# Kernel tuning notes

Measured on AMD Instinct MI355X. Metric: run time of the kernel, lower is better.

Reference implementation:

```python
import jax, jax.numpy as jnp
import numpy as np


def _embedding_distances(dictionary, x_flat):
    # dictionary: [D, C], x_flat: [T, C] -> [T, D]
    dict_norms = jnp.sum(dictionary * dictionary, axis=-1)          # [D]
    x_norms = jnp.sum(x_flat * x_flat, axis=-1)                     # [T]
    dots = jnp.einsum('tc,dc->td', x_flat, dictionary)              # [T, D]
    return -2.0 * dots + dict_norms[None, :] + x_norms[:, None]


def _quantize(x, dictionary):
    # x: [N, C, H, W]
    N, C, H, W = x.shape
    cl = jnp.transpose(x, (0, 2, 3, 1))                             # [N, H, W, C]
    diffs = _embedding_distances(dictionary, cl.reshape(-1, C))     # [NHW, D]
    idxs = jnp.argmin(diffs, axis=-1).reshape(N, H, W)              # [N, H, W]
    embedded = jnp.transpose(dictionary[idxs], (0, 3, 1, 2))        # [N, C, H, W]
    embedded_pt = jax.lax.stop_gradient(embedded) + (x - jax.lax.stop_gradient(x))
    return embedded, embedded_pt, idxs


def setup_inputs() -> dict:
    key = jax.random.key(0)
    k1, k2, k3 = jax.random.split(key, 3)
    N, C, H, W, D = 32, 256, 32, 32, 1024
    return {
        'inputs': jax.random.normal(k1, (N, C, H, W), dtype=jnp.float32),
        'inputs_thermal': jax.random.normal(k2, (N, C, H, W), dtype=jnp.float32),
        'dictionary': jax.random.normal(k3, (D, C), dtype=jnp.float32),
    }


def reference(inputs, inputs_thermal, dictionary):
    embedded, embedded_pt, idxs = _quantize(inputs, dictionary)
    embedded_t, embedded_pt_t, idxs_t = _quantize(inputs_thermal, dictionary)
    return (embedded, embedded_pt, idxs, embedded_t, embedded_pt_t, idxs_t)
```

## Files before the change

kernel.cpp:

```cpp
#include <hip/hip_runtime.h>

#define NB    32
#define CCH   256
#define HW    1024
#define NPIX  (NB*HW)
#define DDICT 1024

#define EMB_ELEMS  ((size_t)NB*CCH*HW)
#define SEC_ELEMS  (2*EMB_ELEMS + NPIX)

#define TPX  256
#define TD   128
#define NDT  (DDICT/TD)
#define BK   32
#define NKC  (CCH/BK)
#define NPH  (NDT*NKC)

#define TAU  0.125f

typedef __attribute__((ext_vector_type(8))) short bf16x8;
typedef __attribute__((ext_vector_type(4))) float f32x4;

__device__ inline ushort split_rne(float f, float& rest) {
    uint u = __float_as_uint(f);
    uint r = u + 0x7FFFu + ((u >> 16) & 1u);
    rest = f - __uint_as_float(r & 0xFFFF0000u);
    return (ushort)(r >> 16);
}

__device__ inline ushort rne_bf16(float f) {
    uint u = __float_as_uint(f);
    return (ushort)((u + 0x7FFFu + ((u >> 16) & 1u)) >> 16);
}

__device__ inline void gll16(const void* g, void* l) {
    __builtin_amdgcn_global_load_lds(
        (const __attribute__((address_space(1))) uint*)g,
        (__attribute__((address_space(3))) uint*)l,
        16, 0, 0);
}

__device__ inline void nts16(float* p, float a, float b, float c, float d) {
    f32x4 v = {a, b, c, d};
    __builtin_nontemporal_store(v, (f32x4*)p);
}

__global__ void dict_norms_kernel(const float* __restrict__ dict,
                                  float* __restrict__ norms,
                                  int* __restrict__ cnts) {
    if (blockIdx.x == 0 && threadIdx.x < 2) cnts[threadIdx.x] = 0;
    int d = blockIdx.x * blockDim.x + threadIdx.x;
    if (d < DDICT) {
        const float4* row = (const float4*)(dict + (size_t)d * CCH);
        float s = 0.f;
#pragma unroll 8
        for (int i = 0; i < CCH / 4; ++i) {
            float4 v = row[i];
            s += v.x * v.x + v.y * v.y + v.z * v.z + v.w * v.w;
        }
        norms[d] = s;
    }
}

__global__ void dict_split_kernel(const float* __restrict__ dict,
                                  ushort* __restrict__ dHs,
                                  ushort* __restrict__ dMs,
                                  float* __restrict__ dictT) {
    int d = blockIdx.x;
    int lane = threadIdx.x;
    float4 f = ((const float4*)(dict + (size_t)d * CCH))[lane];
    float v[4] = {f.x, f.y, f.z, f.w};
    ushort h[4], m[4];
#pragma unroll
    for (int i = 0; i < 4; ++i) {
        float r1;
        h[i] = split_rne(v[i], r1);
        m[i] = rne_bf16(r1);
    }
    int c0 = lane * 4;
    int kc = c0 >> 5, oct = (c0 >> 3) & 3, e0 = c0 & 7;
    int dt = d >> 7, dd = d & 127;
    int slot = (oct + (dd >> 1)) & 3;
    size_t base = ((size_t)(dt * NKC + kc)) * 4096 + dd * 32 + slot * 8 + e0;
    *(ushort4*)(dHs + base) = make_ushort4(h[0], h[1], h[2], h[3]);
    *(ushort4*)(dMs + base) = make_ushort4(m[0], m[1], m[2], m[3]);
#pragma unroll
    for (int j = 0; j < 4; ++j)
        dictT[(size_t)(c0 + j) * DDICT + d] = v[j];
}

__global__ __launch_bounds__(512, 1)
void vq_mfma_kernel(const float* __restrict__ x0,
                    const float* __restrict__ x1,
                    const ushort* __restrict__ dHs,
                    const ushort* __restrict__ dMs,
                    const float* __restrict__ norms,
                    const float* __restrict__ dict,
                    float* __restrict__ out,
                    int* __restrict__ cnts,
                    int* __restrict__ lists) {
    __shared__ ushort Bs[2][2][4096];
    __shared__ float nrm_s[DDICT];
    __shared__ int   idx_s[TPX];

    const int t    = threadIdx.x;
    const int lane = t & 63;
    const int wv   = t >> 6;
    const int lx   = lane & 15;
    const int q    = lane >> 4;
    const int m0w  = wv * 32;
    const int z    = blockIdx.y;

    const int g0  = blockIdx.x * TPX;
    const int n   = g0 / HW;
    const int hw0 = g0 % HW;

    const float* x = z ? x1 : x0;
    float* out_base = out + (size_t)z * SEC_ELEMS;
    float* out_idx  = out_base + 2 * EMB_ELEMS;
    int* cnt  = cnts + z;
    int* list = lists + (size_t)z * NPIX;

    *(float2*)(nrm_s + t * 2) = *(const float2*)(norms + t * 2);

    const float* xbase = x + (size_t)n * CCH * HW + hw0 + m0w + lx;
    bf16x8 Ah[8][2], Am[8][2];
#pragma unroll
    for (int kc = 0; kc < NKC; ++kc) {
        float a_f[2][8];
#pragma unroll
        for (int mi = 0; mi < 2; ++mi)
#pragma unroll
            for (int j = 0; j < 8; ++j)
                a_f[mi][j] = __builtin_nontemporal_load(
                    xbase + (size_t)(kc * BK + q * 8 + j) * HW + mi * 16);
#pragma unroll
        for (int mi = 0; mi < 2; ++mi)
#pragma unroll
            for (int j = 0; j < 8; ++j) {
                float r1;
                ushort h = split_rne(a_f[mi][j], r1);
                Ah[kc][mi][j] = (short)h;
                Am[kc][mi][j] = (short)rne_bf16(r1);
            }
    }

    auto stage = [&](int p, int b) {
#pragma unroll
        for (int plane = 0; plane < 2; ++plane) {
            const ushort* sp = (plane ? dMs : dHs) + (size_t)p * 4096;
            gll16(sp + t * 8, &Bs[b][plane][wv * 512]);
        }
    };

    __syncthreads();
    stage(0, 0);

    float b1r[2][4], b2r[2][4]; int i1r[2][4];
#pragma unroll
    for (int mi = 0; mi < 2; ++mi)
#pragma unroll
        for (int r = 0; r < 4; ++r) {
            b1r[mi][r] = 3.0e38f; b2r[mi][r] = 3.0e38f; i1r[mi][r] = 0;
        }

    for (int dt = 0; dt < NDT; ++dt) {
        f32x4 acc[2][8] = {};
#pragma unroll
        for (int kc = 0; kc < NKC; ++kc) {
            const int p = dt * 8 + kc;
            asm volatile("s_waitcnt vmcnt(0)" ::: "memory");
            __builtin_amdgcn_s_barrier();
            if (p + 1 < NPH) stage(p + 1, (p + 1) & 1);

            const ushort* bb = &Bs[p & 1][0][0];
            __builtin_amdgcn_s_setprio(1);
#pragma unroll
            for (int ni = 0; ni < 8; ++ni) {
                int nn   = ni * 16 + lx;
                int slot = (q + (nn >> 1)) & 3;
                int off  = nn * 32 + slot * 8;
                bf16x8 Bh = *(const bf16x8*)(bb + off);
                bf16x8 Bm = *(const bf16x8*)(bb + 4096 + off);
#pragma unroll
                for (int mi = 0; mi < 2; ++mi) {
                    f32x4 c = acc[mi][ni];
                    c = __builtin_amdgcn_mfma_f32_16x16x32_bf16(Ah[kc][mi], Bh, c, 0, 0, 0);
                    c = __builtin_amdgcn_mfma_f32_16x16x32_bf16(Ah[kc][mi], Bm, c, 0, 0, 0);
                    c = __builtin_amdgcn_mfma_f32_16x16x32_bf16(Am[kc][mi], Bh, c, 0, 0, 0);
                    acc[mi][ni] = c;
                }
            }
            __builtin_amdgcn_s_setprio(0);
        }

        const int d0 = dt * TD;
        float nrm[8];
#pragma unroll
        for (int ni = 0; ni < 8; ++ni) nrm[ni] = nrm_s[d0 + ni * 16 + lx];

#pragma unroll
        for (int mi = 0; mi < 2; ++mi)
#pragma unroll
            for (int r = 0; r < 4; ++r) {
                float c1 = 3.0e38f, c2 = 3.0e38f; int ci = 0;
#pragma unroll
                for (int ni = 0; ni < 8; ++ni) {
                    float dist = fmaf(-2.f, acc[mi][ni][r], nrm[ni]);
                    if (dist < c1)      { c2 = c1; c1 = dist; ci = ni * 16 + lx; }
                    else if (dist < c2) { c2 = dist; }
                }
#pragma unroll
                for (int off = 1; off < 16; off <<= 1) {
                    float o1 = __shfl_xor(c1, off);
                    int   oi = __shfl_xor(ci, off);
                    float o2 = __shfl_xor(c2, off);
                    if (o1 < c1 || (o1 == c1 && oi < ci)) {
                        c2 = fminf(c1, o2); c1 = o1; ci = oi;
                    } else {
                        c2 = fminf(c2, o1);
                    }
                }
                if (c1 < b1r[mi][r]) {
                    b2r[mi][r] = fminf(b1r[mi][r], c2);
                    b1r[mi][r] = c1;
                    i1r[mi][r] = d0 + ci;
                } else {
                    b2r[mi][r] = fminf(b2r[mi][r], c1);
                }
            }
    }

#pragma unroll
    for (int mi = 0; mi < 2; ++mi)
#pragma unroll
        for (int r = 0; r < 4; ++r) {
            if (lx == 0) {
                int loc = m0w + mi * 16 + q * 4 + r;
                int g = g0 + loc;
                idx_s[loc] = i1r[mi][r];
                out_idx[g] = (float)i1r[mi][r];
                if (b2r[mi][r] - b1r[mi][r] < TAU) {
                    int slot = atomicAdd(cnt, 1);
                    list[slot] = g;
                }
            }
        }
    __syncthreads();

    const int pg = t & 63;
    const int cg = t >> 6;
    const int hwp = hw0 + pg * 4;
    const float* r0 = dict + (size_t)idx_s[pg * 4 + 0] * CCH;
    const float* r1 = dict + (size_t)idx_s[pg * 4 + 1] * CCH;
    const float* r2 = dict + (size_t)idx_s[pg * 4 + 2] * CCH;
    const float* r3 = dict + (size_t)idx_s[pg * 4 + 3] * CCH;
    float* oe = out_base;
    float* op = out_base + EMB_ELEMS;
    const size_t obase = (size_t)n * CCH * HW + hwp;

#pragma unroll
    for (int cq = 0; cq < 8; ++cq) {
        int c = cg * 32 + cq * 4;
        float4 q0 = *(const float4*)(r0 + c);
        float4 q1 = *(const float4*)(r1 + c);
        float4 q2 = *(const float4*)(r2 + c);
        float4 q3 = *(const float4*)(r3 + c);
        nts16(oe + obase + (size_t)(c + 0) * HW, q0.x, q1.x, q2.x, q3.x);
        nts16(op + obase + (size_t)(c + 0) * HW, q0.x, q1.x, q2.x, q3.x);
        nts16(oe + obase + (size_t)(c + 1) * HW, q0.y, q1.y, q2.y, q3.y);
        nts16(op + obase + (size_t)(c + 1) * HW, q0.y, q1.y, q2.y, q3.y);
        nts16(oe + obase + (size_t)(c + 2) * HW, q0.z, q1.z, q2.z, q3.z);
        nts16(op + obase + (size_t)(c + 2) * HW, q0.z, q1.z, q2.z, q3.z);
        nts16(oe + obase + (size_t)(c + 3) * HW, q0.w, q1.w, q2.w, q3.w);
        nts16(op + obase + (size_t)(c + 3) * HW, q0.w, q1.w, q2.w, q3.w);
    }
}

__global__ __launch_bounds__(256)
void vq_rescue_kernel(const float* __restrict__ x0,
                      const float* __restrict__ x1,
                      const float* __restrict__ dictT,
                      const float* __restrict__ dict,
                      const float* __restrict__ norms,
                      const int* __restrict__ cnts,
                      const int* __restrict__ lists,
                      float* __restrict__ out) {
    __shared__ float xr[CCH];
    __shared__ float rd_s[4];
    __shared__ int   ri_s[4];
    __shared__ int   bi_s;
    const int z = blockIdx.z;
    const float* x = z ? x1 : x0;
    const int* list = lists + (size_t)z * NPIX;
    float* out_emb    = out + (size_t)z * SEC_ELEMS;
    float* out_emb_pt = out_emb + EMB_ELEMS;
    float* out_idx    = out_emb + 2 * EMB_ELEMS;
    const int t    = threadIdx.x;
    const int lane = t & 63;
    const int wv   = t >> 6;
    const int total = cnts[z];

    for (int w = blockIdx.x; w < total; w += gridDim.x) {
        const int g  = list[w];
        const int n  = g / HW;
        const int hw = g % HW;
        xr[t] = x[(size_t)n * CCH * HW + (size_t)t * HW + hw];
        __syncthreads();

        float bd = 3.0e38f; int bi = 0;
#pragma unroll
        for (int dd = 0; dd < 4; ++dd) {
            int d = dd * 256 + t;
            float dot = 0.f;
#pragma unroll 8
            for (int k = 0; k < CCH; ++k)
                dot = fmaf(xr[k], dictT[(size_t)k * DDICT + d], dot);
            float dist = fmaf(-2.f, dot, norms[d]);
            if (dist < bd) { bd = dist; bi = d; }
        }
#pragma unroll
        for (int off = 1; off < 64; off <<= 1) {
            float od = __shfl_xor(bd, off);
            int   oi = __shfl_xor(bi, off);
            if (od < bd || (od == bd && oi < bi)) { bd = od; bi = oi; }
        }
        if (lane == 0) { rd_s[wv] = bd; ri_s[wv] = bi; }
        __syncthreads();
        if (t == 0) {
            float fb = rd_s[0]; int fi = ri_s[0];
#pragma unroll
            for (int q2 = 1; q2 < 4; ++q2)
                if (rd_s[q2] < fb || (rd_s[q2] == fb && ri_s[q2] < fi)) {
                    fb = rd_s[q2]; fi = ri_s[q2];
                }
            bi_s = fi;
            out_idx[g] = (float)fi;
        }
        __syncthreads();
        float v = dict[(size_t)bi_s * CCH + t];
        size_t o = (size_t)n * CCH * HW + (size_t)t * HW + hw;
        out_emb[o]    = v;
        out_emb_pt[o] = v;
        __syncthreads();
    }
}

extern "C" void kernel_launch(void* const* d_in, const int* in_sizes, int n_in,
                              void* d_out, int out_size, void* d_ws, size_t ws_size,
                              hipStream_t stream) {
    const float* x0   = (const float*)d_in[0];
    const float* x1   = (const float*)d_in[1];
    const float* dict = (const float*)d_in[2];
    float* out = (float*)d_out;

    float*  norms = (float*)d_ws;
    ushort* dHs   = (ushort*)(norms + DDICT);
    ushort* dMs   = dHs + (size_t)DDICT * CCH;
    float*  dictT = (float*)(dMs + (size_t)DDICT * CCH);
    int*    lists = (int*)(dictT + (size_t)DDICT * CCH);
    int*    cnts  = lists + 2 * NPIX;

    dict_norms_kernel<<<dim3(DDICT / 256), dim3(256), 0, stream>>>(dict, norms, cnts);
    dict_split_kernel<<<dim3(DDICT), dim3(64), 0, stream>>>(dict, dHs, dMs, dictT);

    vq_mfma_kernel<<<dim3(NPIX / TPX, 2), dim3(512), 0, stream>>>(
        x0, x1, dHs, dMs, norms, dict, out, cnts, lists);

    vq_rescue_kernel<<<dim3(1024, 1, 2), dim3(256), 0, stream>>>(
        x0, x1, dictT, dict, norms, cnts, lists, out);
}
```

Measured before the change: 430.7 us.

## Batch rescue pixels per block and tighten the rescue margin

The rescue kernel now handles 16 flagged pixels per block. Each dictT load is reused across all 16 pixels through register accumulators, instead of one pixel per block iteration, which cuts dictionary memory traffic in the exact fp32 recheck. The TAU margin drops from 0.125 to 0.05, so fewer pixels are sent to rescue, at some risk of argmin mismatches on near ties. The nontemporal hint on the input loads in the MFMA kernel is also removed, and the grid is reshaped.

```diff
diff --git a/kernel.cpp b/kernel.cpp
--- a/kernel.cpp
+++ b/kernel.cpp
@@ -16,7 +16,9 @@
 #define NKC  (CCH/BK)
 #define NPH  (NDT*NKC)
 
-#define TAU  0.125f
+#define TAU  0.05f
+
+#define RPX  16
 
 typedef __attribute__((ext_vector_type(8))) short bf16x8;
 typedef __attribute__((ext_vector_type(4))) float f32x4;
@@ -132,8 +134,7 @@
         for (int mi = 0; mi < 2; ++mi)
 #pragma unroll
             for (int j = 0; j < 8; ++j)
-                a_f[mi][j] = __builtin_nontemporal_load(
-                    xbase + (size_t)(kc * BK + q * 8 + j) * HW + mi * 16);
+                a_f[mi][j] = xbase[(size_t)(kc * BK + q * 8 + j) * HW + mi * 16];
 #pragma unroll
         for (int mi = 0; mi < 2; ++mi)
 #pragma unroll
@@ -286,11 +287,12 @@
                       const int* __restrict__ cnts,
                       const int* __restrict__ lists,
                       float* __restrict__ out) {
-    __shared__ float xr[CCH];
-    __shared__ float rd_s[4];
-    __shared__ int   ri_s[4];
-    __shared__ int   bi_s;
-    const int z = blockIdx.z;
+    __shared__ float xr[CCH][RPX];
+    __shared__ float rd_s[4][RPX];
+    __shared__ int   ri_s[4][RPX];
+    __shared__ int   gi_s[RPX];
+    __shared__ int   bi_s[RPX];
+    const int z = blockIdx.y;
     const float* x = z ? x1 : x0;
     const int* list = lists + (size_t)z * NPIX;
     float* out_emb    = out + (size_t)z * SEC_ELEMS;
@@ -301,47 +303,88 @@
     const int wv   = t >> 6;
     const int total = cnts[z];
 
-    for (int w = blockIdx.x; w < total; w += gridDim.x) {
-        const int g  = list[w];
-        const int n  = g / HW;
-        const int hw = g % HW;
-        xr[t] = x[(size_t)n * CCH * HW + (size_t)t * HW + hw];
+    for (int w0 = blockIdx.x * RPX; w0 < total; w0 += gridDim.x * RPX) {
+        const int np = min(RPX, total - w0);
+        if (t < RPX) gi_s[t] = list[w0 + ((t < np) ? t : (np - 1))];
         __syncthreads();
 
-        float bd = 3.0e38f; int bi = 0;
-#pragma unroll
-        for (int dd = 0; dd < 4; ++dd) {
-            int d = dd * 256 + t;
-            float dot = 0.f;
-#pragma unroll 8
-            for (int k = 0; k < CCH; ++k)
-                dot = fmaf(xr[k], dictT[(size_t)k * DDICT + d], dot);
-            float dist = fmaf(-2.f, dot, norms[d]);
-            if (dist < bd) { bd = dist; bi = d; }
-        }
-#pragma unroll
-        for (int off = 1; off < 64; off <<= 1) {
-            float od = __shfl_xor(bd, off);
-            int   oi = __shfl_xor(bi, off);
-            if (od < bd || (od == bd && oi < bi)) { bd = od; bi = oi; }
-        }
-        if (lane == 0) { rd_s[wv] = bd; ri_s[wv] = bi; }
+        {
+            const int p  = t >> 4;
+            const int j0 = (t & 15) * 16;
+            const int g  = gi_s[p];
+            const int n  = g / HW, hw = g % HW;
+            const float* xb = x + (size_t)n * CCH * HW + hw;
+#pragma unroll
+            for (int j = 0; j < 16; ++j)
+                xr[j0 + j][p] = xb[(size_t)(j0 + j) * HW];
+        }
         __syncthreads();
-        if (t == 0) {
-            float fb = rd_s[0]; int fi = ri_s[0];
+
+        float acc[4][RPX] = {};
+        for (int k = 0; k < CCH; ++k) {
+            float xp[RPX];
+#pragma unroll
+            for (int p4 = 0; p4 < RPX / 4; ++p4) {
+                f32x4 v = *(const f32x4*)&xr[k][p4 * 4];
+#pragma unroll
+                for (int j = 0; j < 4; ++j) xp[p4 * 4 + j] = v[j];
+            }
+#pragma unroll
+            for (int dd = 0; dd < 4; ++dd) {
+                float v = dictT[(size_t)k * DDICT + dd * 256 + t];
+#pragma unroll
+                for (int p = 0; p < RPX; ++p)
+                    acc[dd][p] = fmaf(xp[p], v, acc[dd][p]);
+            }
+        }
+
+#pragma unroll
+        for (int p = 0; p < RPX; ++p) {
+            float bd = 3.0e38f; int bi = 0;
+#pragma unroll
+            for (int dd = 0; dd < 4; ++dd) {
+                int d = dd * 256 + t;
+                float dist = fmaf(-2.f, acc[dd][p], norms[d]);
+                if (dist < bd) { bd = dist; bi = d; }
+            }
+#pragma unroll
+            for (int off = 1; off < 64; off <<= 1) {
+                float od = __shfl_xor(bd, off);
+                int   oi = __shfl_xor(bi, off);
+                if (od < bd || (od == bd && oi < bi)) { bd = od; bi = oi; }
+            }
+            if (lane == 0) { rd_s[wv][p] = bd; ri_s[wv][p] = bi; }
+        }
+        __syncthreads();
+        if (t < RPX) {
+            const int p = t;
+            float fb = rd_s[0][p]; int fi = ri_s[0][p];
 #pragma unroll
             for (int q2 = 1; q2 < 4; ++q2)
-                if (rd_s[q2] < fb || (rd_s[q2] == fb && ri_s[q2] < fi)) {
-                    fb = rd_s[q2]; fi = ri_s[q2];
-                }
-            bi_s = fi;
-            out_idx[g] = (float)fi;
+                if (rd_s[q2][p] < fb || (rd_s[q2][p] == fb && ri_s[q2][p] < fi)) {
+                    fb = rd_s[q2][p]; fi = ri_s[q2][p];
+                }
+            bi_s[p] = fi;
+            if (p < np) out_idx[gi_s[p]] = (float)fi;
         }
         __syncthreads();
-        float v = dict[(size_t)bi_s * CCH + t];
-        size_t o = (size_t)n * CCH * HW + (size_t)t * HW + hw;
-        out_emb[o]    = v;
-        out_emb_pt[o] = v;
+
+        {
+            const int p  = t >> 4;
+            const int j0 = (t & 15) * 16;
+            if (p < np) {
+                const int g = gi_s[p];
+                const int n = g / HW, hw = g % HW;
+                const float* dr = dict + (size_t)bi_s[p] * CCH;
+                const size_t ob = (size_t)n * CCH * HW + hw;
+#pragma unroll
+                for (int j = 0; j < 16; ++j) {
+                    float v = dr[j0 + j];
+                    out_emb[ob + (size_t)(j0 + j) * HW]    = v;
+                    out_emb_pt[ob + (size_t)(j0 + j) * HW] = v;
+                }
+            }
+        }
         __syncthreads();
     }
 }
@@ -367,6 +410,6 @@
     vq_mfma_kernel<<<dim3(NPIX / TPX, 2), dim3(512), 0, stream>>>(
         x0, x1, dHs, dMs, norms, dict, out, cnts, lists);
 
-    vq_rescue_kernel<<<dim3(1024, 1, 2), dim3(256), 0, stream>>>(
+    vq_rescue_kernel<<<dim3(512, 2), dim3(256), 0, stream>>>(
         x0, x1, dictT, dict, norms, cnts, lists, out);
 }
```

After: 421.0 us. 1.02x faster.
